# Optimization experiments

Measured on AMD Instinct MI355X. Metric: run time of the kernel, lower is better.

## Reference

```python
import jax, jax.numpy as jnp
import numpy as np

B, P, Q, N, D = 64, 12, 12, 1024, 64
DOW, TOD = 7, 288  # day-of-week / time-of-day one-hot depths (GMAN STEmbedding)


def setup_inputs() -> dict:
    key = jax.random.key(0)
    ks = iter(jax.random.split(key, 40))
    def g(shape, scale=0.05):
        return jax.random.normal(next(ks), shape, jnp.float32) * scale
    inp = {
        "X": jax.random.normal(next(ks), (B, P, N), jnp.float32),
        "ZC": jax.random.normal(next(ks), (B, P, 400), jnp.float32),
        "ZF": jax.random.normal(next(ks), (B, P, 1600), jnp.float32),
        "SE": g((N, D)),
        # STEmbedding FCs
        "W_se1": g((D, D)), "b_se1": jnp.zeros((D,), jnp.float32),
        "W_se2": g((D, D)), "b_se2": jnp.zeros((D,), jnp.float32),
        "W_te1": g((DOW + TOD, D)), "b_te1": jnp.zeros((D,), jnp.float32),
        "W_te2": g((D, D)), "b_te2": jnp.zeros((D,), jnp.float32),
        # FC_X_in
        "W_in1": g((1, D)), "b_in1": jnp.zeros((D,), jnp.float32),
        "W_in2": g((D, D)), "b_in2": jnp.zeros((D,), jnp.float32),
        # DCGRU layer 1 (gconv over [x||state, support@(x||state)] -> 4D input)
        "Wg1": g((4 * D, 2 * D)), "bg1": jnp.ones((2 * D,), jnp.float32),
        "Wc1": g((4 * D, D)), "bc1": jnp.zeros((D,), jnp.float32),
        # DCGRU layer 2
        "Wg2": g((4 * D, 2 * D)), "bg2": jnp.ones((2 * D,), jnp.float32),
        "Wc2": g((4 * D, D)), "bc2": jnp.zeros((D,), jnp.float32),
        # FC_X_out
        "W_o1": g((D, D)), "b_o1": jnp.zeros((D,), jnp.float32),
        "W_o2": g((D, Q)), "b_o2": jnp.zeros((Q,), jnp.float32),
        "TE": jax.random.randint(next(ks), (B, P + Q, 2), 0, 7, jnp.int32),
    }
    return inp


def _dcgru_scan(x_seq, support, Wg, bg, Wc, bc):
    """x_seq: [B,P,N,D] -> (sequence [B,P,N,D], last state [B,N,D])."""
    def gconv(x, s, W, b):
        z = jnp.concatenate([x, s], -1)                      # [B,N,2D]
        z1 = jnp.einsum('nm,bmd->bnd', support, z)           # diffusion step K=1
        return jnp.concatenate([z, z1], -1) @ W + b

    def step(state, x_t):
        ru = jax.nn.sigmoid(gconv(x_t, state, Wg, bg))       # [B,N,2D]
        r, u = jnp.split(ru, 2, axis=-1)
        c = jnp.tanh(gconv(x_t, r * state, Wc, bc))
        new = u * state + (1.0 - u) * c
        return new, new

    state0 = jnp.zeros(x_seq.shape[:1] + x_seq.shape[2:], x_seq.dtype)
    last, seq = jax.lax.scan(step, state0, jnp.swapaxes(x_seq, 0, 1))
    return jnp.swapaxes(seq, 0, 1), last


def reference(X, ZC, ZF, SE, W_se1, b_se1, W_se2, b_se2, W_te1, b_te1,
              W_te2, b_te2, W_in1, b_in1, W_in2, b_in2,
              Wg1, bg1, Wc1, bc1, Wg2, bg2, Wc2, bc2,
              W_o1, b_o1, W_o2, b_o2, TE):
    # adjacency is identity in this module; random_walk(I).T == I
    adj = jnp.eye(N, dtype=jnp.float32)
    support = (adj / jnp.sum(adj, axis=1, keepdims=True)).T

    # STEmbedding: spatial + temporal embedding
    se = jax.nn.relu(SE @ W_se1 + b_se1) @ W_se2 + b_se2                 # [N,D]
    te_oh = jnp.concatenate([
        jax.nn.one_hot(TE[..., 0], DOW, dtype=jnp.float32),
        jax.nn.one_hot(TE[..., 1], TOD, dtype=jnp.float32)], -1)        # [B,P+Q,295]
    te = jax.nn.relu(te_oh @ W_te1 + b_te1) @ W_te2 + b_te2              # [B,P+Q,D]
    STEX = (se[None, None] + te[:, :, None, :])[:, :P]                   # [B,P,N,D]

    # FC_X_in on expanded X, add STE
    Xe = X[..., None]                                                    # [B,P,N,1]
    Xe = jax.nn.relu(Xe @ W_in1 + b_in1) @ W_in2 + b_in2                 # [B,P,N,D]
    Xe = Xe + STEX

    seq1, _ = _dcgru_scan(Xe, support, Wg1, bg1, Wc1, bc1)               # [B,P,N,D]
    _, h = _dcgru_scan(seq1, support, Wg2, bg2, Wc2, bc2)                # [B,N,D]

    Y = jax.nn.relu(h @ W_o1 + b_o1) @ W_o2 + b_o2                       # [B,N,Q]
    return jnp.transpose(Y, (0, 2, 1))                                   # [B,Q,N]
```

## Files before the change

kernel.cpp:

```cpp
#include <hip/hip_runtime.h>


#define NB 1024

typedef float f32x4 __attribute__((ext_vector_type(4)));
typedef __bf16 bf16x8 __attribute__((ext_vector_type(8)));
typedef int i32x4 __attribute__((ext_vector_type(4)));

#define MFMA(a, b, c) __builtin_amdgcn_mfma_f32_16x16x32_bf16(a, b, c, 0, 0, 0)

__device__ __forceinline__ float fexp(float x) {
    return __builtin_amdgcn_exp2f(x * 1.44269504088896341f);
}
__device__ __forceinline__ float fsigmoid(float x) {
    return __builtin_amdgcn_rcpf(1.0f + fexp(-x));
}
__device__ __forceinline__ float ftanh(float x) {
    return 1.0f - 2.0f * __builtin_amdgcn_rcpf(1.0f + fexp(2.0f * x));
}

__device__ __forceinline__ bf16x8 ldfrag(const unsigned short* p) {
    i32x4 t = *(const i32x4*)p;
    return __builtin_bit_cast(bf16x8, t);
}
__device__ __forceinline__ void split8(f32x4 a0, f32x4 a1, bf16x8& hi, bf16x8& lo) {
    #pragma unroll
    for (int i = 0; i < 4; i++) {
        __bf16 h0 = (__bf16)a0[i]; hi[i] = h0;     lo[i] = (__bf16)(a0[i] - (float)h0);
        __bf16 h1 = (__bf16)a1[i]; hi[4 + i] = h1; lo[4 + i] = (__bf16)(a1[i] - (float)h1);
    }
}
__device__ __forceinline__ void wsplit(float v, unsigned short* dhi, unsigned short* dlo) {
    __bf16 h = (__bf16)v;
    __bf16 l = (__bf16)(v - (float)h);
    *dhi = __builtin_bit_cast(unsigned short, h);
    *dlo = __builtin_bit_cast(unsigned short, l);
}


__global__ void prep_gates(const float* __restrict__ Wg1, const float* __restrict__ Wg2,
                           unsigned short* __restrict__ fr) {
    int i = blockIdx.x * 256 + threadIdx.x;
    if (i >= 4096) return;
    int layer = i >> 11, r = i & 2047;
    int w = r >> 9; r &= 511; int nt = r >> 8; r &= 255; int ks = r >> 6; int lane = r & 63;
    const float* Wg = layer ? Wg2 : Wg1;
    int n = lane & 15, q = lane >> 4;
    int col = nt ? (64 + w * 16 + n) : (w * 16 + n);
    unsigned short* dst = fr + layer * 32768 + (((w * 2 + nt) * 4 + ks) * 2) * 512 + lane * 8;
    #pragma unroll
    for (int j = 0; j < 8; j++) {
        int k = ks * 32 + q * 8 + j;
        float v = Wg[k * 128 + col] + Wg[(k + 128) * 128 + col];
        wsplit(v, dst + j, dst + 512 + j);
    }
}

__global__ void prep_cand(const float* __restrict__ Wc1, const float* __restrict__ Wc2,
                          unsigned short* __restrict__ fr) {
    int i = blockIdx.x * 256 + threadIdx.x;
    if (i >= 2048) return;
    int layer = i >> 10, r = i & 1023;
    int w = r >> 8; r &= 255; int ks = r >> 6; int lane = r & 63;
    const float* Wc = layer ? Wc2 : Wc1;
    int n = lane & 15, q = lane >> 4;
    int col = w * 16 + n;
    unsigned short* dst = fr + 65536 + layer * 16384 + ((w * 4 + ks) * 2) * 512 + lane * 8;
    #pragma unroll
    for (int j = 0; j < 8; j++) {
        int k = ks * 32 + q * 8 + j;
        float v = Wc[k * 64 + col] + Wc[(k + 128) * 64 + col];
        wsplit(v, dst + j, dst + 512 + j);
    }
}

__global__ void prep_small(const float* __restrict__ Win2, const float* __restrict__ Wo1,
                           unsigned short* __restrict__ fr) {
    int i = blockIdx.x * 256 + threadIdx.x;
    if (i >= 1024) return;
    int kind = i >> 9, r = i & 511;
    int w = r >> 7; r &= 127; int ks = r >> 6; int lane = r & 63;
    const float* W = kind ? Wo1 : Win2;
    int n = lane & 15, q = lane >> 4;
    int col = w * 16 + n;
    unsigned short* dst = fr + 98304 + kind * 8192 + ((w * 2 + ks) * 2) * 512 + lane * 8;
    #pragma unroll
    for (int j = 0; j < 8; j++) {
        int k = ks * 32 + q * 8 + j;
        float v = W[k * 64 + col];
        wsplit(v, dst + j, dst + 512 + j);
    }
}

__global__ void prep_se(const float* __restrict__ SE, const float* __restrict__ W1,
                        const float* __restrict__ b1, const float* __restrict__ W2,
                        const float* __restrict__ b2, const float* __restrict__ bin2,
                        float* __restrict__ seW) {
    __shared__ float h[64];
    int n = blockIdx.x, d = threadIdx.x;
    float acc = b1[d];
    for (int k = 0; k < 64; k++) acc = fmaf(SE[n * 64 + k], W1[k * 64 + d], acc);
    h[d] = fmaxf(acc, 0.0f);
    __syncthreads();
    float acc2 = b2[d];
    for (int k = 0; k < 64; k++) acc2 = fmaf(h[k], W2[k * 64 + d], acc2);
    seW[n * 64 + d] = acc2 + bin2[d];
}

__global__ void prep_te(const int* __restrict__ TE, const float* __restrict__ W1,
                        const float* __restrict__ b1, const float* __restrict__ W2,
                        const float* __restrict__ b2, float* __restrict__ teo) {
    __shared__ float h[64];
    int bp = blockIdx.x;
    int b = bp / 12, p = bp - b * 12;
    int d = threadIdx.x;
    int dow = TE[(b * 24 + p) * 2 + 0];
    int tod = TE[(b * 24 + p) * 2 + 1];
    float v = W1[dow * 64 + d] + W1[(7 + tod) * 64 + d] + b1[d];
    h[d] = fmaxf(v, 0.0f);
    __syncthreads();
    float acc = b2[d];
    for (int k = 0; k < 64; k++) acc = fmaf(h[k], W2[k * 64 + d], acc);
    teo[bp * 64 + d] = acc;
}

#define SW(t, k) ((t) * 64 + ((k) ^ (((t) & 3) << 3)))

__device__ __forceinline__ void gru_layer(
    const float* __restrict__ XIN, float* __restrict__ S, float* __restrict__ RS,
    const unsigned short* __restrict__ frG, const unsigned short* __restrict__ frC,
    const float* __restrict__ bg, const float* __restrict__ bc, int l, int w) {
    const int n16 = l & 15, q = l >> 4;
    const int col = w * 16 + n16;
    f32x4 accR[4], accU[4];
    #pragma unroll
    for (int mt = 0; mt < 4; mt++) { accR[mt] = (f32x4)0.0f; accU[mt] = (f32x4)0.0f; }
    #pragma unroll
    for (int ks = 0; ks < 4; ks++) {
        bf16x8 bhiR = ldfrag(frG + ((0 * 4 + ks) * 2 + 0) * 512 + l * 8);
        bf16x8 bloR = ldfrag(frG + ((0 * 4 + ks) * 2 + 1) * 512 + l * 8);
        bf16x8 bhiU = ldfrag(frG + ((1 * 4 + ks) * 2 + 0) * 512 + l * 8);
        bf16x8 bloU = ldfrag(frG + ((1 * 4 + ks) * 2 + 1) * 512 + l * 8);
        const float* src = (ks < 2) ? XIN : S;
        const int kk = (ks * 32 + q * 8) & 63;
        #pragma unroll
        for (int mt = 0; mt < 4; mt++) {
            const int m = mt * 16 + n16;
            const float* ap = src + m * 64 + (kk ^ ((m & 3) << 3));
            f32x4 a0 = *(const f32x4*)ap, a1 = *(const f32x4*)(ap + 4);
            bf16x8 ahi, alo; split8(a0, a1, ahi, alo);
            accR[mt] = MFMA(ahi, bhiR, accR[mt]);
            accR[mt] = MFMA(alo, bhiR, accR[mt]);
            accR[mt] = MFMA(ahi, bloR, accR[mt]);
            accU[mt] = MFMA(ahi, bhiU, accU[mt]);
            accU[mt] = MFMA(alo, bhiU, accU[mt]);
            accU[mt] = MFMA(ahi, bloU, accU[mt]);
        }
    }
    const float bgr = bg[col];
    #pragma unroll
    for (int mt = 0; mt < 4; mt++)
        #pragma unroll
        for (int r = 0; r < 4; r++) {
            int tok = mt * 16 + q * 4 + r;
            float rs = fsigmoid(accR[mt][r] + bgr) * S[SW(tok, col)];
            RS[SW(tok, col)] = rs;
        }
    __syncthreads();
    f32x4 accC[4];
    #pragma unroll
    for (int mt = 0; mt < 4; mt++) accC[mt] = (f32x4)0.0f;
    #pragma unroll
    for (int ks = 0; ks < 4; ks++) {
        bf16x8 bhi = ldfrag(frC + (ks * 2 + 0) * 512 + l * 8);
        bf16x8 blo = ldfrag(frC + (ks * 2 + 1) * 512 + l * 8);
        const float* src = (ks < 2) ? XIN : RS;
        const int kk = (ks * 32 + q * 8) & 63;
        #pragma unroll
        for (int mt = 0; mt < 4; mt++) {
            const int m = mt * 16 + n16;
            const float* ap = src + m * 64 + (kk ^ ((m & 3) << 3));
            f32x4 a0 = *(const f32x4*)ap, a1 = *(const f32x4*)(ap + 4);
            bf16x8 ahi, alo; split8(a0, a1, ahi, alo);
            accC[mt] = MFMA(ahi, bhi, accC[mt]);
            accC[mt] = MFMA(alo, bhi, accC[mt]);
            accC[mt] = MFMA(ahi, blo, accC[mt]);
        }
    }
    const float bcc = bc[col], bgu = bg[64 + col];
    #pragma unroll
    for (int mt = 0; mt < 4; mt++)
        #pragma unroll
        for (int r = 0; r < 4; r++) {
            int tok = mt * 16 + q * 4 + r;
            float u = fsigmoid(accU[mt][r] + bgu);
            float cnd = ftanh(accC[mt][r] + bcc);
            int a = SW(tok, col);
            S[a] = u * S[a] + (1.0f - u) * cnd;
        }
    __syncthreads();
}

__global__ __launch_bounds__(256, 2) void gman_main(
    const float* __restrict__ X, const float* __restrict__ ws,
    const float* __restrict__ Win1, const float* __restrict__ bin1,
    const float* __restrict__ bg1, const float* __restrict__ bc1,
    const float* __restrict__ bg2, const float* __restrict__ bc2,
    const float* __restrict__ bo1, const float* __restrict__ Wo2,
    const float* __restrict__ bo2, float* __restrict__ out) {
    __shared__ float XE[4096], S1[4096], S2[4096], RS[4096];

    const int tid = threadIdx.x;
    const int l = tid & 63;
    const int w = tid >> 6;
    const int n16 = l & 15, q = l >> 4;
    const int col = w * 16 + n16;
    const int b = blockIdx.x >> 4;
    const int n0 = (blockIdx.x & 15) << 6;

    const unsigned short* frU = (const unsigned short*)ws;
    const unsigned short* frG1 = frU + w * 8192;
    const unsigned short* frG2 = frU + 32768 + w * 8192;
    const unsigned short* frC1 = frU + 65536 + w * 4096;
    const unsigned short* frC2 = frU + 81920 + w * 4096;
    const unsigned short* frX  = frU + 98304 + w * 2048;
    const unsigned short* frH  = frU + 106496 + w * 2048;
    const float* seW = ws + 57344;
    const float* teo = ws + 122880;

    #pragma unroll
    for (int i = 0; i < 16; i++) { S1[tid + i * 256] = 0.0f; S2[tid + i * 256] = 0.0f; }

    #pragma unroll 1
    for (int p = 0; p < 12; p++) {
        if (tid < 64) RS[tid] = X[(b * 12 + p) * NB + n0 + tid];
        __syncthreads();
        f32x4 accX[4];
        #pragma unroll
        for (int mt = 0; mt < 4; mt++) accX[mt] = (f32x4)0.0f;
        #pragma unroll
        for (int ks = 0; ks < 2; ks++) {
            const int k0 = ks * 32 + q * 8;
            f32x4 w1a = *(const f32x4*)(Win1 + k0), w1b = *(const f32x4*)(Win1 + k0 + 4);
            f32x4 b1a = *(const f32x4*)(bin1 + k0), b1b = *(const f32x4*)(bin1 + k0 + 4);
            bf16x8 bhi = ldfrag(frX + (ks * 2 + 0) * 512 + l * 8);
            bf16x8 blo = ldfrag(frX + (ks * 2 + 1) * 512 + l * 8);
            #pragma unroll
            for (int mt = 0; mt < 4; mt++) {
                const float xm = RS[mt * 16 + n16];
                f32x4 h0, h1v;
                #pragma unroll
                for (int i = 0; i < 4; i++) {
                    h0[i]  = fmaxf(fmaf(xm, w1a[i], b1a[i]), 0.0f);
                    h1v[i] = fmaxf(fmaf(xm, w1b[i], b1b[i]), 0.0f);
                }
                bf16x8 ahi, alo; split8(h0, h1v, ahi, alo);
                accX[mt] = MFMA(ahi, bhi, accX[mt]);
                accX[mt] = MFMA(alo, bhi, accX[mt]);
                accX[mt] = MFMA(ahi, blo, accX[mt]);
            }
        }
        const float tev = teo[(b * 12 + p) * 64 + col];
        #pragma unroll
        for (int mt = 0; mt < 4; mt++)
            #pragma unroll
            for (int r = 0; r < 4; r++) {
                int tok = mt * 16 + q * 4 + r;
                XE[SW(tok, col)] = accX[mt][r] + seW[(n0 + tok) * 64 + col] + tev;
            }
        __syncthreads();

        gru_layer(XE, S1, RS, frG1, frC1, bg1, bc1, l, w);
        gru_layer(S1, S2, RS, frG2, frC2, bg2, bc2, l, w);
    }

    f32x4 accH[4];
    #pragma unroll
    for (int mt = 0; mt < 4; mt++) accH[mt] = (f32x4)0.0f;
    #pragma unroll
    for (int ks = 0; ks < 2; ks++) {
        bf16x8 bhi = ldfrag(frH + (ks * 2 + 0) * 512 + l * 8);
        bf16x8 blo = ldfrag(frH + (ks * 2 + 1) * 512 + l * 8);
        const int kk = ks * 32 + q * 8;
        #pragma unroll
        for (int mt = 0; mt < 4; mt++) {
            const int m = mt * 16 + n16;
            const float* ap = S2 + m * 64 + (kk ^ ((m & 3) << 3));
            f32x4 a0 = *(const f32x4*)ap, a1 = *(const f32x4*)(ap + 4);
            bf16x8 ahi, alo; split8(a0, a1, ahi, alo);
            accH[mt] = MFMA(ahi, bhi, accH[mt]);
            accH[mt] = MFMA(alo, bhi, accH[mt]);
            accH[mt] = MFMA(ahi, blo, accH[mt]);
        }
    }
    const float bo = bo1[col];
    #pragma unroll
    for (int mt = 0; mt < 4; mt++)
        #pragma unroll
        for (int r = 0; r < 4; r++) {
            int tok = mt * 16 + q * 4 + r;
            XE[SW(tok, col)] = fmaxf(accH[mt][r] + bo, 0.0f);
        }
    __syncthreads();
    const int uw = __builtin_amdgcn_readfirstlane(w);
    float y0 = bo2[3 * uw], y1 = bo2[3 * uw + 1], y2 = bo2[3 * uw + 2];
    #pragma unroll 8
    for (int j = 0; j < 64; j++) {
        const float hj = XE[SW(l, j)];
        y0 = fmaf(hj, Wo2[j * 12 + 3 * uw + 0], y0);
        y1 = fmaf(hj, Wo2[j * 12 + 3 * uw + 1], y1);
        y2 = fmaf(hj, Wo2[j * 12 + 3 * uw + 2], y2);
    }
    out[(b * 12 + 3 * uw + 0) * NB + n0 + l] = y0;
    out[(b * 12 + 3 * uw + 1) * NB + n0 + l] = y1;
    out[(b * 12 + 3 * uw + 2) * NB + n0 + l] = y2;
}

extern "C" void kernel_launch(void* const* d_in, const int* in_sizes, int n_in,
                              void* d_out, int out_size, void* d_ws, size_t ws_size,
                              hipStream_t stream) {
    const float* X    = (const float*)d_in[0];
    const float* SE   = (const float*)d_in[3];
    const float* Wse1 = (const float*)d_in[4];
    const float* bse1 = (const float*)d_in[5];
    const float* Wse2 = (const float*)d_in[6];
    const float* bse2 = (const float*)d_in[7];
    const float* Wte1 = (const float*)d_in[8];
    const float* bte1 = (const float*)d_in[9];
    const float* Wte2 = (const float*)d_in[10];
    const float* bte2 = (const float*)d_in[11];
    const float* Win1 = (const float*)d_in[12];
    const float* bin1 = (const float*)d_in[13];
    const float* Win2 = (const float*)d_in[14];
    const float* bin2 = (const float*)d_in[15];
    const float* Wg1  = (const float*)d_in[16];
    const float* bg1  = (const float*)d_in[17];
    const float* Wc1  = (const float*)d_in[18];
    const float* bc1  = (const float*)d_in[19];
    const float* Wg2  = (const float*)d_in[20];
    const float* bg2  = (const float*)d_in[21];
    const float* Wc2  = (const float*)d_in[22];
    const float* bc2  = (const float*)d_in[23];
    const float* Wo1  = (const float*)d_in[24];
    const float* bo1  = (const float*)d_in[25];
    const float* Wo2  = (const float*)d_in[26];
    const float* bo2  = (const float*)d_in[27];
    const int*   TE   = (const int*)d_in[28];

    float* ws = (float*)d_ws;
    unsigned short* fr = (unsigned short*)ws;
    float* seW = ws + 57344;
    float* teo = ws + 122880;
    float* out = (float*)d_out;

    prep_gates<<<16, 256, 0, stream>>>(Wg1, Wg2, fr);
    prep_cand<<<8, 256, 0, stream>>>(Wc1, Wc2, fr);
    prep_small<<<4, 256, 0, stream>>>(Win2, Wo1, fr);
    prep_se<<<1024, 64, 0, stream>>>(SE, Wse1, bse1, Wse2, bse2, bin2, seW);
    prep_te<<<768, 64, 0, stream>>>(TE, Wte1, bte1, Wte2, bte2, teo);
    gman_main<<<1024, 256, 0, stream>>>(X, ws, Win1, bin1, bg1, bc1, bg2, bc2,
                                        bo1, Wo2, bo2, out);
}
```

Measured before the change: 669.4 us.

## Fuse x-part of candidate gconv into gate pass, swizzle LDS, register-cache SE

The candidate GEMM's input-half (XIN rows) is now computed in the same loop as the gate GEMMs, so XIN A-fragments are loaded and split once and only the RS half remains after the barrier. The LDS swizzle gains an extra XOR bit and the A loads read the two 4-float halves via the swizzled index to reduce bank conflicts. The spatial embedding is pre-laid out per lane by prep_se and held in registers across timesteps instead of being re-read from global memory each step. The cost is more live accumulator registers (accC held through the gate pass), which may pressure occupancy under launch_bounds(256,2), plus an extra barrier added before the XE write.

After: 580.2 us. -13.3%, faster.

```diff
diff --git a/kernel.cpp b/kernel.cpp
--- a/kernel.cpp
+++ b/kernel.cpp
@@ -95,7 +95,7 @@
 __global__ void prep_se(const float* __restrict__ SE, const float* __restrict__ W1,
                         const float* __restrict__ b1, const float* __restrict__ W2,
                         const float* __restrict__ b2, const float* __restrict__ bin2,
-                        float* __restrict__ seW) {
+                        float* __restrict__ seB) {
     __shared__ float h[64];
     int n = blockIdx.x, d = threadIdx.x;
     float acc = b1[d];
@@ -104,7 +104,10 @@
     __syncthreads();
     float acc2 = b2[d];
     for (int k = 0; k < 64; k++) acc2 = fmaf(h[k], W2[k * 64 + d], acc2);
-    seW[n * 64 + d] = acc2 + bin2[d];
+    int nb = n >> 6, tok = n & 63;
+    int mt = tok >> 4, q = (tok >> 2) & 3, r = tok & 3;
+    int w = d >> 4, n16 = d & 15;
+    seB[(((nb * 4 + w) * 64) + q * 16 + n16) * 16 + mt * 4 + r] = acc2 + bin2[d];
 }
 
 __global__ void prep_te(const int* __restrict__ TE, const float* __restrict__ W1,
@@ -124,7 +127,15 @@
     teo[bp * 64 + d] = acc;
 }
 
-#define SW(t, k) ((t) * 64 + ((k) ^ (((t) & 3) << 3)))
+#define SW(t, k) ((t) * 64 + ((k) ^ (((t) & 3) << 3) ^ ((t) & 4)))
+
+__device__ __forceinline__ void lda_split(const float* __restrict__ src, int m, int k0,
+                                          bf16x8& ahi, bf16x8& alo) {
+    const int sk = (k0 ^ ((m & 3) << 3) ^ (m & 4));
+    f32x4 a0 = *(const f32x4*)(src + m * 64 + sk);
+    f32x4 a1 = *(const f32x4*)(src + m * 64 + (sk ^ 4));
+    split8(a0, a1, ahi, alo);
+}
 
 __device__ __forceinline__ void gru_layer(
     const float* __restrict__ XIN, float* __restrict__ S, float* __restrict__ RS,
@@ -132,29 +143,52 @@
     const float* __restrict__ bg, const float* __restrict__ bc, int l, int w) {
     const int n16 = l & 15, q = l >> 4;
     const int col = w * 16 + n16;
-    f32x4 accR[4], accU[4];
-    #pragma unroll
-    for (int mt = 0; mt < 4; mt++) { accR[mt] = (f32x4)0.0f; accU[mt] = (f32x4)0.0f; }
-    #pragma unroll
-    for (int ks = 0; ks < 4; ks++) {
+    f32x4 accR[4], accU[4], accC[4];
+    #pragma unroll
+    for (int mt = 0; mt < 4; mt++) {
+        accR[mt] = (f32x4)0.0f; accU[mt] = (f32x4)0.0f; accC[mt] = (f32x4)0.0f;
+    }
+    #pragma unroll
+    for (int ks = 0; ks < 2; ks++) {
         bf16x8 bhiR = ldfrag(frG + ((0 * 4 + ks) * 2 + 0) * 512 + l * 8);
         bf16x8 bloR = ldfrag(frG + ((0 * 4 + ks) * 2 + 1) * 512 + l * 8);
         bf16x8 bhiU = ldfrag(frG + ((1 * 4 + ks) * 2 + 0) * 512 + l * 8);
         bf16x8 bloU = ldfrag(frG + ((1 * 4 + ks) * 2 + 1) * 512 + l * 8);
-        const float* src = (ks < 2) ? XIN : S;
-        const int kk = (ks * 32 + q * 8) & 63;
+        bf16x8 bhiC = ldfrag(frC + (ks * 2 + 0) * 512 + l * 8);
+        bf16x8 bloC = ldfrag(frC + (ks * 2 + 1) * 512 + l * 8);
+        const int kk = ks * 32 + q * 8;
         #pragma unroll
         for (int mt = 0; mt < 4; mt++) {
-            const int m = mt * 16 + n16;
-            const float* ap = src + m * 64 + (kk ^ ((m & 3) << 3));
-            f32x4 a0 = *(const f32x4*)ap, a1 = *(const f32x4*)(ap + 4);
-            bf16x8 ahi, alo; split8(a0, a1, ahi, alo);
+            bf16x8 ahi, alo;
+            lda_split(XIN, mt * 16 + n16, kk, ahi, alo);
             accR[mt] = MFMA(ahi, bhiR, accR[mt]);
             accR[mt] = MFMA(alo, bhiR, accR[mt]);
             accR[mt] = MFMA(ahi, bloR, accR[mt]);
             accU[mt] = MFMA(ahi, bhiU, accU[mt]);
             accU[mt] = MFMA(alo, bhiU, accU[mt]);
             accU[mt] = MFMA(ahi, bloU, accU[mt]);
+            accC[mt] = MFMA(ahi, bhiC, accC[mt]);
+            accC[mt] = MFMA(alo, bhiC, accC[mt]);
+            accC[mt] = MFMA(ahi, bloC, accC[mt]);
+        }
+    }
+    #pragma unroll
+    for (int ks = 2; ks < 4; ks++) {
+        bf16x8 bhiR = ldfrag(frG + ((0 * 4 + ks) * 2 + 0) * 512 + l * 8);
+        bf16x8 bloR = ldfrag(frG + ((0 * 4 + ks) * 2 + 1) * 512 + l * 8);
+        bf16x8 bhiU = ldfrag(frG + ((1 * 4 + ks) * 2 + 0) * 512 + l * 8);
+        bf16x8 bloU = ldfrag(frG + ((1 * 4 + ks) * 2 + 1) * 512 + l * 8);
+        const int kk = (ks - 2) * 32 + q * 8;
+        #pragma unroll
+        for (int mt = 0; mt < 4; mt++) {
+            bf16x8 ahi, alo;
+            lda_split(S, mt * 16 + n16, kk, ahi, alo);
+            accR[mt] = MFMA(ahi, bhiR, accR[mt]);
+            accR[mt] = MFMA(alo, bhiR, accR[mt]);
+            accR[mt] = MFMA(ahi, bloR, accR[mt]);
+            accU[mt] = MFMA(ahi, bhiU, accU[mt]);
+            accU[mt] = MFMA(alo, bhiU, accU[mt]);
+            accU[mt] = MFMA(ahi, bloU, accU[mt]);
         }
     }
     const float bgr = bg[col];
@@ -163,25 +197,18 @@
         #pragma unroll
         for (int r = 0; r < 4; r++) {
             int tok = mt * 16 + q * 4 + r;
-            float rs = fsigmoid(accR[mt][r] + bgr) * S[SW(tok, col)];
-            RS[SW(tok, col)] = rs;
-        }
-    __syncthreads();
-    f32x4 accC[4];
-    #pragma unroll
-    for (int mt = 0; mt < 4; mt++) accC[mt] = (f32x4)0.0f;
-    #pragma unroll
-    for (int ks = 0; ks < 4; ks++) {
+            RS[SW(tok, col)] = fsigmoid(accR[mt][r] + bgr) * S[SW(tok, col)];
+        }
+    __syncthreads();
+    #pragma unroll
+    for (int ks = 2; ks < 4; ks++) {
         bf16x8 bhi = ldfrag(frC + (ks * 2 + 0) * 512 + l * 8);
         bf16x8 blo = ldfrag(frC + (ks * 2 + 1) * 512 + l * 8);
-        const float* src = (ks < 2) ? XIN : RS;
-        const int kk = (ks * 32 + q * 8) & 63;
+        const int kk = (ks - 2) * 32 + q * 8;
         #pragma unroll
         for (int mt = 0; mt < 4; mt++) {
-            const int m = mt * 16 + n16;
-            const float* ap = src + m * 64 + (kk ^ ((m & 3) << 3));
-            f32x4 a0 = *(const f32x4*)ap, a1 = *(const f32x4*)(ap + 4);
-            bf16x8 ahi, alo; split8(a0, a1, ahi, alo);
+            bf16x8 ahi, alo;
+            lda_split(RS, mt * 16 + n16, kk, ahi, alo);
             accC[mt] = MFMA(ahi, bhi, accC[mt]);
             accC[mt] = MFMA(alo, bhi, accC[mt]);
             accC[mt] = MFMA(ahi, blo, accC[mt]);
@@ -216,7 +243,8 @@
     const int n16 = l & 15, q = l >> 4;
     const int col = w * 16 + n16;
     const int b = blockIdx.x >> 4;
-    const int n0 = (blockIdx.x & 15) << 6;
+    const int nb = blockIdx.x & 15;
+    const int n0 = nb << 6;
 
     const unsigned short* frU = (const unsigned short*)ws;
     const unsigned short* frG1 = frU + w * 8192;
@@ -225,11 +253,15 @@
     const unsigned short* frC2 = frU + 81920 + w * 4096;
     const unsigned short* frX  = frU + 98304 + w * 2048;
     const unsigned short* frH  = frU + 106496 + w * 2048;
-    const float* seW = ws + 57344;
+    const float* seQ = ws + 57344 + (((nb * 4 + w) * 64) + l) * 16;
     const float* teo = ws + 122880;
 
     #pragma unroll
     for (int i = 0; i < 16; i++) { S1[tid + i * 256] = 0.0f; S2[tid + i * 256] = 0.0f; }
+
+    f32x4 se[4];
+    #pragma unroll
+    for (int mt = 0; mt < 4; mt++) se[mt] = *(const f32x4*)(seQ + mt * 4);
 
     #pragma unroll 1
     for (int p = 0; p < 12; p++) {
@@ -261,12 +293,13 @@
             }
         }
         const float tev = teo[(b * 12 + p) * 64 + col];
+        __syncthreads();
         #pragma unroll
         for (int mt = 0; mt < 4; mt++)
             #pragma unroll
             for (int r = 0; r < 4; r++) {
                 int tok = mt * 16 + q * 4 + r;
-                XE[SW(tok, col)] = accX[mt][r] + seW[(n0 + tok) * 64 + col] + tev;
+                XE[SW(tok, col)] = accX[mt][r] + se[mt][r] + tev;
             }
         __syncthreads();
 
@@ -284,10 +317,8 @@
         const int kk = ks * 32 + q * 8;
         #pragma unroll
         for (int mt = 0; mt < 4; mt++) {
-            const int m = mt * 16 + n16;
-            const float* ap = S2 + m * 64 + (kk ^ ((m & 3) << 3));
-            f32x4 a0 = *(const f32x4*)ap, a1 = *(const f32x4*)(ap + 4);
-            bf16x8 ahi, alo; split8(a0, a1, ahi, alo);
+            bf16x8 ahi, alo;
+            lda_split(S2, mt * 16 + n16, kk, ahi, alo);
             accH[mt] = MFMA(ahi, bhi, accH[mt]);
             accH[mt] = MFMA(alo, bhi, accH[mt]);
             accH[mt] = MFMA(ahi, blo, accH[mt]);
@@ -349,14 +380,14 @@
 
     float* ws = (float*)d_ws;
     unsigned short* fr = (unsigned short*)ws;
-    float* seW = ws + 57344;
+    float* seB = ws + 57344;
     float* teo = ws + 122880;
     float* out = (float*)d_out;
 
     prep_gates<<<16, 256, 0, stream>>>(Wg1, Wg2, fr);
     prep_cand<<<8, 256, 0, stream>>>(Wc1, Wc2, fr);
     prep_small<<<4, 256, 0, stream>>>(Win2, Wo1, fr);
-    prep_se<<<1024, 64, 0, stream>>>(SE, Wse1, bse1, Wse2, bse2, bin2, seW);
+    prep_se<<<1024, 64, 0, stream>>>(SE, Wse1, bse1, Wse2, bse2, bin2, seB);
     prep_te<<<768, 64, 0, stream>>>(TE, Wte1, bte1, Wte2, bte2, teo);
     gman_main<<<1024, 256, 0, stream>>>(X, ws, Win1, bin1, bg1, bc1, bg2, bc2,
                                         bo1, Wo2, bo2, out);
```
